# Optimization experiments

Measured on AMD Instinct MI355X. Metric: run time of the kernel, lower is better.

The kernel has to match this reference:

```python
import jax, jax.numpy as jnp
import numpy as np


def setup_inputs() -> dict:
    key = jax.random.key(0)
    k1, k2, k3, k4 = jax.random.split(key, 4)
    B, L, H, E = 2, 10000, 8, 64
    NE = 160000
    return {
        "queries": jax.random.normal(k1, (B, L, H, E), dtype=jnp.float32),
        "keys": jax.random.normal(k2, (B, L, H, E), dtype=jnp.float32),
        "values": jax.random.normal(k3, (B, L, H, E), dtype=jnp.float32),
        "adj": jax.random.randint(k4, (2, NE), 0, L, dtype=jnp.int64),
    }


def reference(queries, keys, values, adj):
    # queries/keys/values: [B, L, H, E]; adj: [2, NE] (row 0 = dst group, row 1 = src)
    B, L, H, E = queries.shape
    softmax_temp = 1.0 / (E ** 0.5)
    dst = adj[0]
    src = adj[1]

    # edge-gather dot product: qk[b, e, h] = sum_d q[b, dst[e], h, d] * k[b, src[e], h, d]
    qk = jnp.sum(queries[:, dst] * keys[:, src], axis=-1) * softmax_temp  # [B, NE, H]

    # segment softmax grouped by destination node (dropout is identity at eval)
    qk_e = qk.transpose(1, 0, 2)  # [NE, B, H] (segment ops act on leading axis)
    seg_max = jax.ops.segment_max(qk_e, dst, num_segments=L)  # [L, B, H]
    ex = jnp.exp(qk_e - seg_max[dst])
    seg_sum = jax.ops.segment_sum(ex, dst, num_segments=L)  # [L, B, H]
    alpha = ex / (seg_sum[dst] + 1e-16)  # [NE, B, H]

    # spmm: gather v at src, weight by alpha, scatter-add to dst
    weighted = values[:, src] * alpha.transpose(1, 0, 2)[..., None]  # [B, NE, H, E]
    out = jnp.zeros_like(values).at[:, dst].add(weighted)  # [B, L, H, E]
    return out
```

## Files before the change

### kernel.cpp

```cpp
#include <hip/hip_runtime.h>

#define BB 2
#define HH 8
#define EE 64
#define ROW (HH * EE)
#define CHUNK 8

__device__ inline unsigned short f2bf(float f) {
  unsigned int u = __float_as_uint(f);
  u = (u + 0x7fffu + ((u >> 16) & 1u)) >> 16;
  return (unsigned short)u;
}

__global__ __launch_bounds__(256) void convert_hist_kernel(
    const float* __restrict__ k, const float* __restrict__ v,
    unsigned short* __restrict__ kbf, unsigned short* __restrict__ vbf,
    const int* __restrict__ dst, int* __restrict__ counts,
    int n4, int NE) {
  int i = blockIdx.x * blockDim.x + threadIdx.x;
  if (i < n4) {
    float4 kf = ((const float4*)k)[i];
    float4 vf = ((const float4*)v)[i];
    ((ushort4*)kbf)[i] = make_ushort4(f2bf(kf.x), f2bf(kf.y), f2bf(kf.z), f2bf(kf.w));
    ((ushort4*)vbf)[i] = make_ushort4(f2bf(vf.x), f2bf(vf.y), f2bf(vf.z), f2bf(vf.w));
  }
  if (i < NE) {
    atomicAdd(&counts[dst[i]], 1);
  }
}

__global__ __launch_bounds__(1024) void scan_kernel(
    const int* __restrict__ counts_in, int* __restrict__ counts_mut,
    int* __restrict__ offsets, int L) {
  __shared__ int sums[1024];
  int tid = threadIdx.x;
  int chunk = (L + 1023) / 1024;
  int beg = tid * chunk;
  int end = min(beg + chunk, L);
  int s = 0;
  for (int i = beg; i < end; ++i) s += counts_in[i];
  sums[tid] = s;
  __syncthreads();
  for (int off = 1; off < 1024; off <<= 1) {
    int val = 0;
    if (tid >= off) val = sums[tid - off];
    __syncthreads();
    if (tid >= off) sums[tid] += val;
    __syncthreads();
  }
  int run = (tid > 0) ? sums[tid - 1] : 0;
  for (int i = beg; i < end; ++i) {
    offsets[i] = run;
    run += counts_in[i];
    counts_mut[i] = 0;
  }
  if (tid == 1023) offsets[L] = run;
}

__global__ __launch_bounds__(256) void fill_csr_kernel(
    const int* __restrict__ dst, const int* __restrict__ src,
    const int* __restrict__ offsets, int* __restrict__ cursor,
    int* __restrict__ csr_src, int NE) {
  int e = blockIdx.x * blockDim.x + threadIdx.x;
  if (e >= NE) return;
  int d = dst[e];
  int pos = atomicAdd(&cursor[d], 1);
  csr_src[offsets[d] + pos] = src[e];
}

__device__ inline void bf8_unpack(uint4 u, float* f) {
  f[0] = __uint_as_float(u.x << 16);
  f[1] = __uint_as_float(u.x & 0xffff0000u);
  f[2] = __uint_as_float(u.y << 16);
  f[3] = __uint_as_float(u.y & 0xffff0000u);
  f[4] = __uint_as_float(u.z << 16);
  f[5] = __uint_as_float(u.z & 0xffff0000u);
  f[6] = __uint_as_float(u.w << 16);
  f[7] = __uint_as_float(u.w & 0xffff0000u);
}

__global__ __launch_bounds__(256) void fused_attn_kernel(
    const float* __restrict__ q, const unsigned short* __restrict__ kbf,
    const unsigned short* __restrict__ vbf, const int* __restrict__ offsets,
    const int* __restrict__ csr_src, float* __restrict__ out, int L) {
  int wid = blockIdx.x * (blockDim.x >> 6) + (threadIdx.x >> 6);
  int lane = threadIdx.x & 63;
  if (wid >= L * BB) return;
  int d = wid >> 1;
  int b = wid & 1;
  int beg = offsets[d];
  int end = offsets[d + 1];

  const float4* qrow = (const float4*)(q + ((size_t)b * L + d) * ROW);
  float4 q0 = qrow[lane * 2 + 0];
  float4 q1 = qrow[lane * 2 + 1];

  float m = -INFINITY;
  float l_run = 0.0f;
  float acc[8];
#pragma unroll
  for (int i = 0; i < 8; ++i) acc[i] = 0.0f;

  const uint4* kb_base = (const uint4*)(kbf + (size_t)b * L * ROW);
  const uint4* vb_base = (const uint4*)(vbf + (size_t)b * L * ROW);

  for (int t0 = beg; t0 < end; t0 += CHUNK) {
    int cnt = min(CHUNK, end - t0);
    uint4 kk[CHUNK], vv[CHUNK];
#pragma unroll
    for (int i = 0; i < CHUNK; ++i) {
      if (i < cnt) {
        int s = csr_src[t0 + i];
        kk[i] = kb_base[(size_t)s * (ROW / 8) + lane];
        vv[i] = vb_base[(size_t)s * (ROW / 8) + lane];
      }
    }
    float qk[CHUNK];
    float cmax = -INFINITY;
#pragma unroll
    for (int i = 0; i < CHUNK; ++i) {
      qk[i] = -INFINITY;
      if (i < cnt) {
        float kf[8];
        bf8_unpack(kk[i], kf);
        float p = q0.x * kf[0] + q0.y * kf[1] + q0.z * kf[2] + q0.w * kf[3] +
                  q1.x * kf[4] + q1.y * kf[5] + q1.z * kf[6] + q1.w * kf[7];
        p += __shfl_xor(p, 1);
        p += __shfl_xor(p, 2);
        p += __shfl_xor(p, 4);
        p *= 0.125f;
        qk[i] = p;
        cmax = fmaxf(cmax, p);
      }
    }
    float mnew = fmaxf(m, cmax);
    float scale = __expf(m - mnew);
    l_run *= scale;
#pragma unroll
    for (int i = 0; i < 8; ++i) acc[i] *= scale;
    m = mnew;
#pragma unroll
    for (int i = 0; i < CHUNK; ++i) {
      if (i < cnt) {
        float a = __expf(qk[i] - m);
        l_run += a;
        float vf[8];
        bf8_unpack(vv[i], vf);
#pragma unroll
        for (int j = 0; j < 8; ++j) acc[j] += a * vf[j];
      }
    }
  }
  float r = 1.0f / (l_run + 1e-16f);
  float4* orow = (float4*)(out + ((size_t)b * L + d) * ROW);
  orow[lane * 2 + 0] = make_float4(acc[0] * r, acc[1] * r, acc[2] * r, acc[3] * r);
  orow[lane * 2 + 1] = make_float4(acc[4] * r, acc[5] * r, acc[6] * r, acc[7] * r);
}

extern "C" void kernel_launch(void* const* d_in, const int* in_sizes, int n_in,
                              void* d_out, int out_size, void* d_ws, size_t ws_size,
                              hipStream_t stream) {
  const float* q = (const float*)d_in[0];
  const float* k = (const float*)d_in[1];
  const float* v = (const float*)d_in[2];
  const int* adj = (const int*)d_in[3];

  const int NE = in_sizes[3] / 2;
  const int L = in_sizes[0] / (BB * HH * EE);
  const int* dst = adj;
  const int* src = adj + NE;
  const int nelem = BB * L * HH * EE;

  char* ws = (char*)d_ws;
  size_t off = 0;
  unsigned short* kbf = (unsigned short*)(ws + off); off += (size_t)nelem * 2;
  unsigned short* vbf = (unsigned short*)(ws + off); off += (size_t)nelem * 2;
  int* counts = (int*)(ws + off);   off += (size_t)L * 4;
  int* offsets = (int*)(ws + off);  off += (size_t)(L + 1) * 4;
  int* csr_src = (int*)(ws + off);  off += (size_t)NE * 4;

  hipMemsetAsync(counts, 0, (size_t)L * 4, stream);

  int n4 = nelem / 4;
  convert_hist_kernel<<<(n4 + 255) / 256, 256, 0, stream>>>(
      k, v, kbf, vbf, dst, counts, n4, NE);

  scan_kernel<<<1, 1024, 0, stream>>>(counts, counts, offsets, L);

  fill_csr_kernel<<<(NE + 255) / 256, 256, 0, stream>>>(
      dst, src, offsets, counts, csr_src, NE);

  int nwaves = L * BB;
  fused_attn_kernel<<<(nwaves + 3) / 4, 256, 0, stream>>>(
      q, kbf, vbf, offsets, csr_src, (float*)d_out, L);
}
```

Baseline: 283.7 us.

## Interleave K/V bf16 rows and use persistent atomic-ticket scheduling

Stores the bf16 K and V rows interleaved in one buffer, so each gathered source node's K and V sit in one contiguous 2 KB row and share locality. The attention kernel becomes persistent: a fixed grid of waves pulls (node, batch) tasks from an atomic ticket counter to balance uneven degrees. The edge loop is split into a full-chunk fast path without per-element predicates and a predicated tail. The cost is one atomic per task, and the ticket is zeroed by extending the counts memset.

```diff
diff --git a/kernel.cpp b/kernel.cpp
--- a/kernel.cpp
+++ b/kernel.cpp
@@ -4,6 +4,7 @@
 #define HH 8
 #define EE 64
 #define ROW (HH * EE)
+#define KVROW (2 * ROW)
 #define CHUNK 8
 
 __device__ inline unsigned short f2bf(float f) {
@@ -14,15 +15,18 @@
 
 __global__ __launch_bounds__(256) void convert_hist_kernel(
     const float* __restrict__ k, const float* __restrict__ v,
-    unsigned short* __restrict__ kbf, unsigned short* __restrict__ vbf,
+    unsigned short* __restrict__ kv,
     const int* __restrict__ dst, int* __restrict__ counts,
     int n4, int NE) {
   int i = blockIdx.x * blockDim.x + threadIdx.x;
   if (i < n4) {
     float4 kf = ((const float4*)k)[i];
     float4 vf = ((const float4*)v)[i];
-    ((ushort4*)kbf)[i] = make_ushort4(f2bf(kf.x), f2bf(kf.y), f2bf(kf.z), f2bf(kf.w));
-    ((ushort4*)vbf)[i] = make_ushort4(f2bf(vf.x), f2bf(vf.y), f2bf(vf.z), f2bf(vf.w));
+    int row = i >> 7;
+    int p4 = i & 127;
+    ushort4* kvrow = (ushort4*)(kv + (size_t)row * KVROW);
+    kvrow[p4]       = make_ushort4(f2bf(kf.x), f2bf(kf.y), f2bf(kf.z), f2bf(kf.w));
+    kvrow[128 + p4] = make_ushort4(f2bf(vf.x), f2bf(vf.y), f2bf(vf.z), f2bf(vf.w));
   }
   if (i < NE) {
     atomicAdd(&counts[dst[i]], 1);
@@ -79,48 +83,52 @@
   f[7] = __uint_as_float(u.w & 0xffff0000u);
 }
 
-__global__ __launch_bounds__(256) void fused_attn_kernel(
-    const float* __restrict__ q, const unsigned short* __restrict__ kbf,
-    const unsigned short* __restrict__ vbf, const int* __restrict__ offsets,
-    const int* __restrict__ csr_src, float* __restrict__ out, int L) {
-  int wid = blockIdx.x * (blockDim.x >> 6) + (threadIdx.x >> 6);
+__global__ __launch_bounds__(256, 4) void fused_attn_kernel(
+    const float* __restrict__ q, const unsigned short* __restrict__ kv,
+    const int* __restrict__ offsets, const int* __restrict__ csr_src,
+    int* __restrict__ ticket, float* __restrict__ out, int L) {
   int lane = threadIdx.x & 63;
-  if (wid >= L * BB) return;
-  int d = wid >> 1;
-  int b = wid & 1;
-  int beg = offsets[d];
-  int end = offsets[d + 1];
-
-  const float4* qrow = (const float4*)(q + ((size_t)b * L + d) * ROW);
-  float4 q0 = qrow[lane * 2 + 0];
-  float4 q1 = qrow[lane * 2 + 1];
-
-  float m = -INFINITY;
-  float l_run = 0.0f;
-  float acc[8];
-#pragma unroll
-  for (int i = 0; i < 8; ++i) acc[i] = 0.0f;
-
-  const uint4* kb_base = (const uint4*)(kbf + (size_t)b * L * ROW);
-  const uint4* vb_base = (const uint4*)(vbf + (size_t)b * L * ROW);
-
-  for (int t0 = beg; t0 < end; t0 += CHUNK) {
-    int cnt = min(CHUNK, end - t0);
-    uint4 kk[CHUNK], vv[CHUNK];
-#pragma unroll
-    for (int i = 0; i < CHUNK; ++i) {
-      if (i < cnt) {
-        int s = csr_src[t0 + i];
-        kk[i] = kb_base[(size_t)s * (ROW / 8) + lane];
-        vv[i] = vb_base[(size_t)s * (ROW / 8) + lane];
-      }
-    }
-    float qk[CHUNK];
-    float cmax = -INFINITY;
-#pragma unroll
-    for (int i = 0; i < CHUNK; ++i) {
-      qk[i] = -INFINITY;
-      if (i < cnt) {
+  const int ntask = L * BB;
+
+  for (;;) {
+    int task;
+    if (lane == 0) task = atomicAdd(ticket, 1);
+    task = __shfl(task, 0);
+    if (task >= ntask) return;
+
+    int d = task >> 1;
+    int b = task & 1;
+    int beg = offsets[d];
+    int end = offsets[d + 1];
+
+    const float4* qrow = (const float4*)(q + ((size_t)b * L + d) * ROW);
+    float4 q0 = qrow[lane * 2 + 0];
+    float4 q1 = qrow[lane * 2 + 1];
+
+    float m = -INFINITY;
+    float l_run = 0.0f;
+    float acc[8];
+#pragma unroll
+    for (int i = 0; i < 8; ++i) acc[i] = 0.0f;
+
+    const uint4* kv_base = (const uint4*)(kv + (size_t)b * L * KVROW);
+
+    int t = beg;
+    for (; t + CHUNK <= end; t += CHUNK) {
+      int srcs[CHUNK];
+#pragma unroll
+      for (int i = 0; i < CHUNK; ++i) srcs[i] = csr_src[t + i];
+      uint4 kk[CHUNK], vv[CHUNK];
+#pragma unroll
+      for (int i = 0; i < CHUNK; ++i) {
+        const uint4* row = kv_base + (size_t)srcs[i] * (KVROW / 8);
+        kk[i] = row[lane];
+        vv[i] = row[64 + lane];
+      }
+      float qk[CHUNK];
+      float cmax = -INFINITY;
+#pragma unroll
+      for (int i = 0; i < CHUNK; ++i) {
         float kf[8];
         bf8_unpack(kk[i], kf);
         float p = q0.x * kf[0] + q0.y * kf[1] + q0.z * kf[2] + q0.w * kf[3] +
@@ -132,16 +140,14 @@
         qk[i] = p;
         cmax = fmaxf(cmax, p);
       }
-    }
-    float mnew = fmaxf(m, cmax);
-    float scale = __expf(m - mnew);
-    l_run *= scale;
-#pragma unroll
-    for (int i = 0; i < 8; ++i) acc[i] *= scale;
-    m = mnew;
-#pragma unroll
-    for (int i = 0; i < CHUNK; ++i) {
-      if (i < cnt) {
+      float mnew = fmaxf(m, cmax);
+      float scale = __expf(m - mnew);
+      l_run *= scale;
+#pragma unroll
+      for (int i = 0; i < 8; ++i) acc[i] *= scale;
+      m = mnew;
+#pragma unroll
+      for (int i = 0; i < CHUNK; ++i) {
         float a = __expf(qk[i] - m);
         l_run += a;
         float vf[8];
@@ -150,11 +156,61 @@
         for (int j = 0; j < 8; ++j) acc[j] += a * vf[j];
       }
     }
-  }
-  float r = 1.0f / (l_run + 1e-16f);
-  float4* orow = (float4*)(out + ((size_t)b * L + d) * ROW);
-  orow[lane * 2 + 0] = make_float4(acc[0] * r, acc[1] * r, acc[2] * r, acc[3] * r);
-  orow[lane * 2 + 1] = make_float4(acc[4] * r, acc[5] * r, acc[6] * r, acc[7] * r);
+    int cnt = end - t;
+    if (cnt > 0) {
+      uint4 kk[CHUNK], vv[CHUNK];
+      int srcs[CHUNK];
+#pragma unroll
+      for (int i = 0; i < CHUNK; ++i) {
+        if (i < cnt) {
+          srcs[i] = csr_src[t + i];
+          const uint4* row = kv_base + (size_t)srcs[i] * (KVROW / 8);
+          kk[i] = row[lane];
+          vv[i] = row[64 + lane];
+        }
+      }
+      float qk[CHUNK];
+      float cmax = -INFINITY;
+#pragma unroll
+      for (int i = 0; i < CHUNK; ++i) {
+        qk[i] = -INFINITY;
+        if (i < cnt) {
+          float kf[8];
+          bf8_unpack(kk[i], kf);
+          float p = q0.x * kf[0] + q0.y * kf[1] + q0.z * kf[2] + q0.w * kf[3] +
+                    q1.x * kf[4] + q1.y * kf[5] + q1.z * kf[6] + q1.w * kf[7];
+          p += __shfl_xor(p, 1);
+          p += __shfl_xor(p, 2);
+          p += __shfl_xor(p, 4);
+          p *= 0.125f;
+          qk[i] = p;
+          cmax = fmaxf(cmax, p);
+        }
+      }
+      float mnew = fmaxf(m, cmax);
+      float scale = __expf(m - mnew);
+      l_run *= scale;
+#pragma unroll
+      for (int i = 0; i < 8; ++i) acc[i] *= scale;
+      m = mnew;
+#pragma unroll
+      for (int i = 0; i < CHUNK; ++i) {
+        if (i < cnt) {
+          float a = __expf(qk[i] - m);
+          l_run += a;
+          float vf[8];
+          bf8_unpack(vv[i], vf);
+#pragma unroll
+          for (int j = 0; j < 8; ++j) acc[j] += a * vf[j];
+        }
+      }
+    }
+
+    float r = 1.0f / (l_run + 1e-16f);
+    float4* orow = (float4*)(out + ((size_t)b * L + d) * ROW);
+    orow[lane * 2 + 0] = make_float4(acc[0] * r, acc[1] * r, acc[2] * r, acc[3] * r);
+    orow[lane * 2 + 1] = make_float4(acc[4] * r, acc[5] * r, acc[6] * r, acc[7] * r);
+  }
 }
 
 extern "C" void kernel_launch(void* const* d_in, const int* in_sizes, int n_in,
@@ -173,24 +229,24 @@
 
   char* ws = (char*)d_ws;
   size_t off = 0;
-  unsigned short* kbf = (unsigned short*)(ws + off); off += (size_t)nelem * 2;
-  unsigned short* vbf = (unsigned short*)(ws + off); off += (size_t)nelem * 2;
+  unsigned short* kvbf = (unsigned short*)(ws + off); off += (size_t)nelem * 2 * 2;
   int* counts = (int*)(ws + off);   off += (size_t)L * 4;
+  int* ticket = (int*)(ws + off);   off += 4;
   int* offsets = (int*)(ws + off);  off += (size_t)(L + 1) * 4;
   int* csr_src = (int*)(ws + off);  off += (size_t)NE * 4;
 
-  hipMemsetAsync(counts, 0, (size_t)L * 4, stream);
+  hipMemsetAsync(counts, 0, (size_t)(L + 1) * 4, stream);
 
   int n4 = nelem / 4;
   convert_hist_kernel<<<(n4 + 255) / 256, 256, 0, stream>>>(
-      k, v, kbf, vbf, dst, counts, n4, NE);
+      k, v, kvbf, dst, counts, n4, NE);
 
   scan_kernel<<<1, 1024, 0, stream>>>(counts, counts, offsets, L);
 
   fill_csr_kernel<<<(NE + 255) / 256, 256, 0, stream>>>(
       dst, src, offsets, counts, csr_src, NE);
 
-  int nwaves = L * BB;
-  fused_attn_kernel<<<(nwaves + 3) / 4, 256, 0, stream>>>(
-      q, kbf, vbf, offsets, csr_src, (float*)d_out, L);
-}
+  int nblocks = 256 * 5;
+  fused_attn_kernel<<<nblocks, 256, 0, stream>>>(
+      q, kvbf, offsets, csr_src, ticket, (float*)d_out, L);
+}
```

Result: slower. 487.2 us (+71.7%).
